# Kernel tuning notes

Hardware: AMD Instinct MI355X
Metric: run time of the kernel (lower is better)

The kernel has to match this reference:

```python
import jax, jax.numpy as jnp
import numpy as np

B = 2; D0 = 41; H = 200; W = 176
C_IN = 128; C_MID = 64
N_PER = 15000; N = B * N_PER
EPS = 1e-3  # spconv BatchNorm1d eps=0.001


def bn_relu(x, valid, gamma, beta):
    # BatchNorm1d (training mode) over ACTIVE voxels only, then ReLU; invalid rows zeroed
    m = valid.astype(x.dtype)[:, None]
    cnt = jnp.maximum(m.sum(), 1.0)
    mean = (x * m).sum(0) / cnt
    var = (((x - mean) ** 2) * m).sum(0) / cnt
    y = gamma * (x - mean) * jax.lax.rsqrt(var + EPS) + beta
    return jnp.maximum(y, 0.0) * m


def build_idx_map(coords, valid, D):
    # dense voxel -> row-index map (-1 = inactive); invalid rows routed out-of-bounds and dropped
    n = coords.shape[0]
    oob = jnp.array([B, D, H, W], jnp.int32)
    c = jnp.where(valid[:, None], coords, oob)
    idx = jnp.full((B, D, H, W), -1, jnp.int32)
    return idx.at[c[:, 0], c[:, 1], c[:, 2], c[:, 3]].set(
        jnp.arange(n, dtype=jnp.int32), mode='drop')


def subm_conv3(feats, coords, valid, idx_map, weight):
    # submanifold 3x3x3 conv: gather active neighbors, GEMM per kernel offset, accumulate
    D = idx_map.shape[1]
    b, z, y, x = coords[:, 0], coords[:, 1], coords[:, 2], coords[:, 3]
    out = jnp.zeros((feats.shape[0], weight.shape[-1]), feats.dtype)
    for dz in (-1, 0, 1):
        for dy in (-1, 0, 1):
            for dx in (-1, 0, 1):
                nz, ny, nx = z + dz, y + dy, x + dx
                inb = valid & (nz >= 0) & (nz < D) & (ny >= 0) & (ny < H) \
                      & (nx >= 0) & (nx < W)
                j = idx_map[b, jnp.clip(nz, 0, D - 1),
                            jnp.clip(ny, 0, H - 1), jnp.clip(nx, 0, W - 1)]
                ok = inb & (j >= 0)
                g = jnp.where(ok[:, None], feats[jnp.clip(j, 0)], 0.0)
                out = out + g @ weight[dz + 1, dy + 1, dx + 1]
    return out


def sparse_conv_z(feats, coords, valid, D, weight):
    # regular SparseConv3d kernel (3,1,1), stride (2,1,1), pad 0: scatter-GEMM into unique outputs
    Dout = (D - 3) // 2 + 1
    b, z, y, x = coords[:, 0], coords[:, 1], coords[:, 2], coords[:, 3]
    sent = B * Dout * H * W  # sentinel linear id (> any valid id)
    cap = 2 * feats.shape[0] + 1  # each input hits <= 2 outputs, + sentinel slot
    lins, vals = [], []
    for kz in range(3):
        t = z - kz
        oz = t // 2
        ok = valid & (t >= 0) & (t % 2 == 0) & (oz < Dout)
        lin = ((b * Dout + oz) * H + y) * W + x
        lins.append(jnp.where(ok, lin, sent))
        vals.append(feats @ weight[kz])
    lin_all = jnp.concatenate(lins)
    val_all = jnp.concatenate(vals)
    uniq = jnp.unique(lin_all, size=cap, fill_value=sent)
    seg = jnp.searchsorted(uniq, lin_all)
    out = jax.ops.segment_sum(val_all, seg, num_segments=cap)
    new_valid = uniq != sent
    lin = jnp.where(new_valid, uniq, 0)
    nb = lin // (Dout * H * W)
    r = lin % (Dout * H * W)
    nz = r // (H * W)
    ny = (r % (H * W)) // W
    nx = r % W
    new_coords = jnp.stack([nb, nz, ny, nx], 1).astype(jnp.int32)
    return out, new_coords, new_valid, Dout


def forward(voxel_features, coors, batch_size,
            w_subm0, g0, b0, w_s1, gs1, bs1,
            w_subm1a, g1a, b1a, w_subm1b, g1b, b1b, w_s2, gs2, bs2):
    v0 = jnp.ones((voxel_features.shape[0],), bool)
    idx0 = build_idx_map(coors, v0, D0)
    x = subm_conv3(voxel_features, coors, v0, idx0, w_subm0)   # 128 -> 64, subm0
    x = bn_relu(x, v0, g0, b0)
    x, c1, v1, D1 = sparse_conv_z(x, coors, v0, D0, w_s1)      # D: 41 -> 20
    x = bn_relu(x, v1, gs1, bs1)
    idx1 = build_idx_map(c1, v1, D1)
    x = bn_relu(subm_conv3(x, c1, v1, idx1, w_subm1a), v1, g1a, b1a)  # subm1
    x = bn_relu(subm_conv3(x, c1, v1, idx1, w_subm1b), v1, g1b, b1b)
    x, c2, v2, D2 = sparse_conv_z(x, c1, v1, D1, w_s2)         # D: 20 -> 9
    x = bn_relu(x, v2, gs2, bs2)
    oob = jnp.array([B, D2, H, W], jnp.int32)
    c2s = jnp.where(v2[:, None], c2, oob)
    dense = jnp.zeros((B, D2, H, W, C_MID), x.dtype)
    dense = dense.at[c2s[:, 0], c2s[:, 1], c2s[:, 2], c2s[:, 3]].set(x, mode='drop')
    dense = dense.transpose(0, 4, 1, 2, 3)                     # [B, C, D2, H, W]
    return dense.reshape(B, C_MID * D2, H, W)


def setup_inputs() -> dict:
    key = jax.random.key(0)
    ks = jax.random.split(key, 6)
    rng = np.random.default_rng(0)
    rows = []
    for b in range(B):
        lin = rng.choice(D0 * H * W, N_PER, replace=False)
        z = lin // (H * W); y = (lin % (H * W)) // W; x = lin % W
        rows.append(np.stack([np.full(N_PER, b), z, y, x], 1))
    coors = jnp.asarray(np.concatenate(rows), jnp.int32)
    s0 = 1.0 / np.sqrt(27.0 * C_IN)
    s1 = 1.0 / np.sqrt(27.0 * C_MID)
    sz = 1.0 / np.sqrt(3.0 * C_MID)
    ones = jnp.ones((C_MID,), jnp.float32)
    zeros = jnp.zeros((C_MID,), jnp.float32)
    return {
        'voxel_features': jax.random.normal(ks[0], (N, C_IN), jnp.float32),
        'coors': coors,
        'batch_size': B,
        'w_subm0': jax.random.normal(ks[1], (3, 3, 3, C_IN, C_MID), jnp.float32) * s0,
        'g0': ones, 'b0': zeros,
        'w_s1': jax.random.normal(ks[2], (3, C_MID, C_MID), jnp.float32) * sz,
        'gs1': ones, 'bs1': zeros,
        'w_subm1a': jax.random.normal(ks[3], (3, 3, 3, C_MID, C_MID), jnp.float32) * s1,
        'g1a': ones, 'b1a': zeros,
        'w_subm1b': jax.random.normal(ks[4], (3, 3, 3, C_MID, C_MID), jnp.float32) * s1,
        'g1b': ones, 'b1b': zeros,
        'w_s2': jax.random.normal(ks[5], (3, C_MID, C_MID), jnp.float32) * sz,
        'gs2': ones, 'bs2': zeros,
    }


def reference(voxel_features, coors, batch_size,
              w_subm0, g0, b0, w_s1, gs1, bs1,
              w_subm1a, g1a, b1a, w_subm1b, g1b, b1b, w_s2, gs2, bs2):
    return forward(voxel_features, coors, batch_size,
                   w_subm0, g0, b0, w_s1, gs1, bs1,
                   w_subm1a, g1a, b1a, w_subm1b, g1b, b1b, w_s2, gs2, bs2)
```

## Files before the change

### kernel.cpp

```cpp
#include <hip/hip_runtime.h>

typedef unsigned short u16;
typedef unsigned int u32;
typedef unsigned long long u64;
typedef __attribute__((ext_vector_type(8))) short bf16x8;
typedef __attribute__((ext_vector_type(4))) float f32x4;

#define H_ 200
#define W_ 176
#define HW_ (200 * 176)
#define D0_ 41
#define D1_ 20
#define D2_ 9
#define B_ 2

__device__ __forceinline__ u16 f2bf(float f) {
  union { float f; u32 u; } c; c.f = f;
  u32 u = c.u;
  u32 r = (u + 0x7fffu + ((u >> 16) & 1u)) >> 16;
  return (u16)r;
}

__global__ void k_boot1(int* __restrict__ ctrl, float* __restrict__ stats,
                        uint4* __restrict__ fillp, int nfill16, int N) {
  int t = blockIdx.x * 256 + threadIdx.x;
  if (t < nfill16) {
    uint4 v;
    v.x = 0xFFFFFFFFu; v.y = 0xFFFFFFFFu; v.z = 0xFFFFFFFFu; v.w = 0xFFFFFFFFu;
    fillp[t] = v;
    return;
  }
  t -= nfill16;
  if (t < 3) ctrl[t] = (t == 0) ? N : 0;
  else if (t < 3 + 2560) stats[t - 3] = 0.f;
}

__device__ __forceinline__ void repack1(const float* __restrict__ w, u16* __restrict__ frag,
                                        int K, int t) {
  int j = t & 7;
  int lane = (t >> 3) & 63;
  int nt = (t >> 9) & 3;
  int rest = t >> 11;
  int KS = K / 32;
  int ks = rest % KS;
  int o = rest / KS;
  int k = ks * 32 + (lane >> 4) * 8 + j;
  int n = nt * 16 + (lane & 15);
  frag[t] = f2bf(w[((size_t)o * K + k) * 64 + n]);
}

__global__ void k_boot2(const float* __restrict__ feats, const float* __restrict__ w0s,
                        const float* __restrict__ w1as, const float* __restrict__ w1bs,
                        const float* __restrict__ wz1s, const float* __restrict__ wz2s,
                        const int* __restrict__ coors,
                        u16* __restrict__ fb, u16* __restrict__ wf0, u16* __restrict__ wf1a,
                        u16* __restrict__ wf1b, u16* __restrict__ wfz1, u16* __restrict__ wfz2,
                        int* __restrict__ idx0, int N) {
  int t = blockIdx.x * 256 + threadIdx.x;
  int NC = N * 128;
  if (t < NC) { fb[t] = f2bf(feats[t]); return; }
  t -= NC;
  if (t < 221184) { repack1(w0s, wf0, 128, t); return; }
  t -= 221184;
  if (t < 110592) { repack1(w1as, wf1a, 64, t); return; }
  t -= 110592;
  if (t < 110592) { repack1(w1bs, wf1b, 64, t); return; }
  t -= 110592;
  if (t < 12288) { repack1(wz1s, wfz1, 64, t); return; }
  t -= 12288;
  if (t < 12288) { repack1(wz2s, wfz2, 64, t); return; }
  t -= 12288;
  if (t < N) {
    int b = coors[t * 4], z = coors[t * 4 + 1], y = coors[t * 4 + 2], x = coors[t * 4 + 3];
    idx0[((size_t)(b * D0_ + z) * H_ + y) * W_ + x] = t;
  }
}

__device__ __forceinline__ void claim_ep(int t, int base64, int cnt,
                                         const int* __restrict__ coordsIn,
                                         const int* __restrict__ idxin, int Din, int Dout,
                                         int* __restrict__ claim, int* __restrict__ coords_out,
                                         int* __restrict__ nbrzN, int* __restrict__ outcnt) {
  int i = base64 + t;
  bool w0 = false, w1 = false;
  int pos0 = 0, pos1 = 0, oz0 = -1, oz1 = -1;
  int b = 0, z = 0, yy = 0, xx = 0;
  if (i < cnt) {
    int4 cc = *(const int4*)(coordsIn + (size_t)i * 4);
    b = cc.x; z = cc.y; yy = cc.z; xx = cc.w;
    if (z & 1) {
      int oz = (z - 1) >> 1;
      if (oz < Dout) oz0 = oz;
    } else {
      int oz = z >> 1;
      if (oz < Dout) oz0 = oz;
      if (z >= 2) oz1 = oz - 1;
    }
    if (oz0 >= 0) {
      pos0 = ((b * Dout + oz0) * H_ + yy) * W_ + xx;
      w0 = (atomicCAS(&claim[pos0], -1, -2) == -1);
    }
    if (oz1 >= 0) {
      pos1 = ((b * Dout + oz1) * H_ + yy) * W_ + xx;
      w1 = (atomicCAS(&claim[pos1], -1, -2) == -1);
    }
  }
  u64 m0 = __ballot(w0), m1 = __ballot(w1);
  int c0 = __popcll(m0), c1 = __popcll(m1);
  int lane = t & 63;
  u64 lt = (lane == 63) ? 0x7FFFFFFFFFFFFFFFull : ((1ull << lane) - 1ull);
  int bse2 = 0;
  if (lane == 0 && (c0 + c1) > 0) bse2 = atomicAdd(outcnt, c0 + c1);
  bse2 = __shfl(bse2, 0);
  if (w0) {
    int id = bse2 + __popcll(m0 & lt);
    claim[pos0] = id;
    coords_out[id * 4 + 0] = b; coords_out[id * 4 + 1] = oz0;
    coords_out[id * 4 + 2] = yy; coords_out[id * 4 + 3] = xx;
    size_t bse = ((size_t)(b * Din + 2 * oz0) * H_ + yy) * W_ + xx;
    nbrzN[id * 3 + 0] = idxin[bse];
    nbrzN[id * 3 + 1] = idxin[bse + HW_];
    nbrzN[id * 3 + 2] = idxin[bse + 2 * (size_t)HW_];
  }
  if (w1) {
    int id = bse2 + c0 + __popcll(m1 & lt);
    claim[pos1] = id;
    coords_out[id * 4 + 0] = b; coords_out[id * 4 + 1] = oz1;
    coords_out[id * 4 + 2] = yy; coords_out[id * 4 + 3] = xx;
    size_t bse = ((size_t)(b * Din + 2 * oz1) * H_ + yy) * W_ + xx;
    nbrzN[id * 3 + 0] = idxin[bse];
    nbrzN[id * 3 + 1] = idxin[bse + HW_];
    nbrzN[id * 3 + 2] = idxin[bse + 2 * (size_t)HW_];
  }
}

__global__ __launch_bounds__(256) void k_conv0(const u16* __restrict__ feats,
                                               const int* __restrict__ coords,
                                               const int* __restrict__ idxmap,
                                               const u16* __restrict__ wfrag,
                                               float* __restrict__ out, int cnt,
                                               float* __restrict__ statsL,
                                               int* __restrict__ claim, int* __restrict__ coords_out,
                                               int* __restrict__ nbrzN, int* __restrict__ outcnt) {
  constexpr int KS = 4;
  __shared__ int snbr[1728];
  __shared__ u32 smask[4];
  __shared__ float lsum[64], lss[64];
  int t = threadIdx.x;
  if (t < 64) { lsum[t] = 0.f; lss[t] = 0.f; }
  if (t < 4) smask[t] = 0;
  __syncthreads();
  int blockBase = blockIdx.x * 64;
  for (int r = t; r < 1728; r += 256) {
    int g = r / 432;
    int rr = r - g * 432;
    int o = rr >> 4;
    int i = blockBase + g * 16 + (rr & 15);
    int j = -1;
    if (i < cnt) {
      int4 cc = *(const int4*)(coords + (size_t)i * 4);
      int nz = cc.y + o / 9 - 1, ny = cc.z + (o / 3) % 3 - 1, nx = cc.w + o % 3 - 1;
      if ((u32)nz < (u32)D0_ && (u32)ny < (u32)H_ && (u32)nx < (u32)W_)
        j = idxmap[((size_t)(cc.x * D0_ + nz) * H_ + ny) * W_ + nx];
    }
    snbr[r] = j;
    if (j >= 0) atomicOr(&smask[g], 1u << o);
  }
  __syncthreads();
  int lane = t & 63;
  int wg = t >> 6;
  int base = blockBase + wg * 16;
  int am = lane & 15, kr = lane >> 4;
  f32x4 acc0 = {0.f, 0.f, 0.f, 0.f};
  f32x4 acc1 = acc0, acc2 = acc0, acc3 = acc0;
  if (base < cnt) {
    u32 mask = smask[wg];
    const int* nb = snbr + wg * 432 + am;
    bf16x8 zf = {0, 0, 0, 0, 0, 0, 0, 0};
    bf16x8 a[KS], an[KS];
    if (mask) {
      int o = __builtin_ctz(mask); mask &= mask - 1;
      int j = nb[o * 16];
#pragma unroll
      for (int ks = 0; ks < KS; ++ks)
        a[ks] = (j >= 0) ? *(const bf16x8*)(feats + (size_t)j * 128 + ks * 32 + kr * 8) : zf;
      while (true) {
        int on = -1, jn = -1;
        if (mask) { on = __builtin_ctz(mask); mask &= mask - 1; jn = nb[on * 16]; }
#pragma unroll
        for (int ks = 0; ks < KS; ++ks)
          an[ks] = (jn >= 0) ? *(const bf16x8*)(feats + (size_t)jn * 128 + ks * 32 + kr * 8) : zf;
        const u16* bw = wfrag + (size_t)o * (KS * 2048) + lane * 8;
#pragma unroll
        for (int ks = 0; ks < KS; ++ks) {
          const u16* bwk = bw + ks * 2048;
          acc0 = __builtin_amdgcn_mfma_f32_16x16x32_bf16(a[ks], *(const bf16x8*)(bwk), acc0, 0, 0, 0);
          acc1 = __builtin_amdgcn_mfma_f32_16x16x32_bf16(a[ks], *(const bf16x8*)(bwk + 512), acc1, 0, 0, 0);
          acc2 = __builtin_amdgcn_mfma_f32_16x16x32_bf16(a[ks], *(const bf16x8*)(bwk + 1024), acc2, 0, 0, 0);
          acc3 = __builtin_amdgcn_mfma_f32_16x16x32_bf16(a[ks], *(const bf16x8*)(bwk + 1536), acc3, 0, 0, 0);
        }
        if (on < 0) break;
        o = on;
#pragma unroll
        for (int ks = 0; ks < KS; ++ks) a[ks] = an[ks];
      }
    }
    float s0 = 0.f, s1 = 0.f, s2 = 0.f, s3 = 0.f;
    float q0 = 0.f, q1 = 0.f, q2 = 0.f, q3 = 0.f;
#pragma unroll
    for (int r = 0; r < 4; ++r) {
      int po = base + kr * 4 + r;
      if (po < cnt) {
        float* op = out + (size_t)po * 64 + am;
        op[0] = acc0[r]; op[16] = acc1[r]; op[32] = acc2[r]; op[48] = acc3[r];
        s0 += acc0[r]; q0 += acc0[r] * acc0[r];
        s1 += acc1[r]; q1 += acc1[r] * acc1[r];
        s2 += acc2[r]; q2 += acc2[r] * acc2[r];
        s3 += acc3[r]; q3 += acc3[r] * acc3[r];
      }
    }
    atomicAdd(&lsum[am], s0); atomicAdd(&lss[am], q0);
    atomicAdd(&lsum[am + 16], s1); atomicAdd(&lss[am + 16], q1);
    atomicAdd(&lsum[am + 32], s2); atomicAdd(&lss[am + 32], q2);
    atomicAdd(&lsum[am + 48], s3); atomicAdd(&lss[am + 48], q3);
  }
  __syncthreads();
  if (t < 64) {
    float s = lsum[t], q = lss[t];
    if (s != 0.f || q != 0.f) {
      float* dst = statsL + (blockIdx.x & 3) * 128;
      atomicAdd(&dst[t], s);
      atomicAdd(&dst[64 + t], q);
    }
    claim_ep(t, blockBase, cnt, coords, idxmap, D0_, D1_, claim, coords_out, nbrzN, outcnt);
  }
}

__device__ __forceinline__ void bn_pre(const float* __restrict__ statsIn, int cntN,
                                       const float* __restrict__ gamma,
                                       const float* __restrict__ beta,
                                       float* __restrict__ ggs, float* __restrict__ bbs, int t) {
  if (t < 64) {
    float s = 0.f, q = 0.f;
#pragma unroll
    for (int k = 0; k < 4; ++k) { s += statsIn[k * 128 + t]; q += statsIn[k * 128 + 64 + t]; }
    float cf = (float)(cntN > 0 ? cntN : 1);
    float mean = s / cf;
    float var = q / cf - mean * mean;
    float inv = rsqrtf(var + 1e-3f);
    float g = gamma[t] * inv;
    ggs[t] = g;
    bbs[t] = beta[t] - mean * g;
  }
}

__global__ __launch_bounds__(256) void k_convz(
    const float* __restrict__ xp, const int* __restrict__ nbrz_in,
    const u16* __restrict__ wfrag, const float* __restrict__ statsIn,
    const int* __restrict__ cntNormP, const float* __restrict__ gamma,
    const float* __restrict__ beta, float* __restrict__ out, const int* __restrict__ cntp,
    float* __restrict__ statsOut,
    const int* __restrict__ coordsL, const int* __restrict__ idxL, int DL,
    int* __restrict__ nbrT, u32* __restrict__ gmaskT,
    int Dnext, int* __restrict__ claimN, int* __restrict__ coordsN,
    int* __restrict__ nbrzN, int* __restrict__ cntN2) {
  int cnt = *cntp;
  int blockBase = blockIdx.x * 64;
  if (blockBase >= cnt) return;
  __shared__ float lsum[64], lss[64], ggs[64], bbs[64];
  __shared__ u32 smask[4];
  int t = threadIdx.x;
  if (t < 64) { lsum[t] = 0.f; lss[t] = 0.f; }
  if (t < 4) smask[t] = 0;
  bn_pre(statsIn, *cntNormP, gamma, beta, ggs, bbs, t);
  __syncthreads();
  if (nbrT) {
    for (int r = t; r < 1728; r += 256) {
      int g = r / 432;
      int rr = r - g * 432;
      int o = rr >> 4;
      int i = blockBase + g * 16 + (rr & 15);
      int j = -1;
      if (i < cnt) {
        int4 cc = *(const int4*)(coordsL + (size_t)i * 4);
        int nz = cc.y + o / 9 - 1, ny = cc.z + (o / 3) % 3 - 1, nx = cc.w + o % 3 - 1;
        if ((u32)nz < (u32)DL && (u32)ny < (u32)H_ && (u32)nx < (u32)W_)
          j = idxL[((size_t)(cc.x * DL + nz) * H_ + ny) * W_ + nx];
      }
      nbrT[(size_t)(blockIdx.x * 4 + g) * 432 + rr] = j;
      if (j >= 0) atomicOr(&smask[g], 1u << o);
    }
  }
  int lane = t & 63;
  int wg = t >> 6;
  int base = blockBase + wg * 16;
  int am = lane & 15, kr = lane >> 4;
  float gr_[16], br_[16];
#pragma unroll
  for (int ks = 0; ks < 2; ++ks)
#pragma unroll
    for (int e = 0; e < 8; ++e) {
      int c = ks * 32 + kr * 8 + e;
      gr_[ks * 8 + e] = ggs[c];
      br_[ks * 8 + e] = bbs[c];
    }
  f32x4 acc0 = {0.f, 0.f, 0.f, 0.f};
  f32x4 acc1 = acc0, acc2 = acc0, acc3 = acc0;
  if (base < cnt) {
    int pt = base + am;
    bool vpt = pt < cnt;
    const int* np = nbrz_in + (size_t)pt * 3;
    bf16x8 zf = {0, 0, 0, 0, 0, 0, 0, 0};
    bf16x8 a[2], an[2];
    auto buildA = [&](int j, bf16x8* aa) {
      if (j >= 0) {
        const float* src = xp + (size_t)j * 64 + kr * 8;
#pragma unroll
        for (int ks = 0; ks < 2; ++ks) {
          float4 v0 = *(const float4*)(src + ks * 32);
          float4 v1 = *(const float4*)(src + ks * 32 + 4);
          bf16x8 w;
          w[0] = (short)f2bf(fmaxf(v0.x * gr_[ks * 8 + 0] + br_[ks * 8 + 0], 0.f));
          w[1] = (short)f2bf(fmaxf(v0.y * gr_[ks * 8 + 1] + br_[ks * 8 + 1], 0.f));
          w[2] = (short)f2bf(fmaxf(v0.z * gr_[ks * 8 + 2] + br_[ks * 8 + 2], 0.f));
          w[3] = (short)f2bf(fmaxf(v0.w * gr_[ks * 8 + 3] + br_[ks * 8 + 3], 0.f));
          w[4] = (short)f2bf(fmaxf(v1.x * gr_[ks * 8 + 4] + br_[ks * 8 + 4], 0.f));
          w[5] = (short)f2bf(fmaxf(v1.y * gr_[ks * 8 + 5] + br_[ks * 8 + 5], 0.f));
          w[6] = (short)f2bf(fmaxf(v1.z * gr_[ks * 8 + 6] + br_[ks * 8 + 6], 0.f));
          w[7] = (short)f2bf(fmaxf(v1.w * gr_[ks * 8 + 7] + br_[ks * 8 + 7], 0.f));
          aa[ks] = w;
        }
      } else { aa[0] = zf; aa[1] = zf; }
    };
    int j = vpt ? np[0] : -1;
    buildA(j, a);
    for (int o = 0; o < 3; ++o) {
      int jn = (o + 1 < 3 && vpt) ? np[o + 1] : -1;
      buildA(jn, an);
      const u16* bw = wfrag + (size_t)o * 4096 + lane * 8;
#pragma unroll
      for (int ks = 0; ks < 2; ++ks) {
        const u16* bwk = bw + ks * 2048;
        acc0 = __builtin_amdgcn_mfma_f32_16x16x32_bf16(a[ks], *(const bf16x8*)(bwk), acc0, 0, 0, 0);
        acc1 = __builtin_amdgcn_mfma_f32_16x16x32_bf16(a[ks], *(const bf16x8*)(bwk + 512), acc1, 0, 0, 0);
        acc2 = __builtin_amdgcn_mfma_f32_16x16x32_bf16(a[ks], *(const bf16x8*)(bwk + 1024), acc2, 0, 0, 0);
        acc3 = __builtin_amdgcn_mfma_f32_16x16x32_bf16(a[ks], *(const bf16x8*)(bwk + 1536), acc3, 0, 0, 0);
      }
      a[0] = an[0]; a[1] = an[1];
    }
    float s0 = 0.f, s1 = 0.f, s2 = 0.f, s3 = 0.f;
    float q0 = 0.f, q1 = 0.f, q2 = 0.f, q3 = 0.f;
#pragma unroll
    for (int r = 0; r < 4; ++r) {
      int po = base + kr * 4 + r;
      if (po < cnt) {
        float* op = out + (size_t)po * 64 + am;
        op[0] = acc0[r]; op[16] = acc1[r]; op[32] = acc2[r]; op[48] = acc3[r];
        s0 += acc0[r]; q0 += acc0[r] * acc0[r];
        s1 += acc1[r]; q1 += acc1[r] * acc1[r];
        s2 += acc2[r]; q2 += acc2[r] * acc2[r];
        s3 += acc3[r]; q3 += acc3[r] * acc3[r];
      }
    }
    atomicAdd(&lsum[am], s0); atomicAdd(&lss[am], q0);
    atomicAdd(&lsum[am + 16], s1); atomicAdd(&lss[am + 16], q1);
    atomicAdd(&lsum[am + 32], s2); atomicAdd(&lss[am + 32], q2);
    atomicAdd(&lsum[am + 48], s3); atomicAdd(&lss[am + 48], q3);
  }
  __syncthreads();
  if (nbrT && t < 4) gmaskT[blockIdx.x * 4 + t] = smask[t];
  if (t < 64) {
    float s = lsum[t], q = lss[t];
    if (s != 0.f || q != 0.f) {
      float* dst = statsOut + (blockIdx.x & 3) * 128;
      atomicAdd(&dst[t], s);
      atomicAdd(&dst[64 + t], q);
    }
    if (claimN)
      claim_ep(t, blockBase, cnt, coordsL, idxL, DL, Dnext, claimN, coordsN, nbrzN, cntN2);
  }
}

__global__ __launch_bounds__(256) void k_conv1(
    const float* __restrict__ xp, const int* __restrict__ nbrT, const u32* __restrict__ gmaskT,
    const u16* __restrict__ wfrag, const float* __restrict__ statsIn,
    const int* __restrict__ cntNormP, const float* __restrict__ gamma,
    const float* __restrict__ beta, float* __restrict__ out, const int* __restrict__ cntp,
    float* __restrict__ statsOut) {
  int cnt = *cntp;
  int blockBase = blockIdx.x * 64;
  if (blockBase >= cnt) return;
  __shared__ float lsum[64], lss[64], ggs[64], bbs[64];
  int t = threadIdx.x;
  if (t < 64) { lsum[t] = 0.f; lss[t] = 0.f; }
  bn_pre(statsIn, *cntNormP, gamma, beta, ggs, bbs, t);
  __syncthreads();
  int lane = t & 63;
  int wg = t >> 6;
  int g = blockIdx.x * 4 + wg;
  int base = blockBase + wg * 16;
  int am = lane & 15, kr = lane >> 4;
  float gr_[16], br_[16];
#pragma unroll
  for (int ks = 0; ks < 2; ++ks)
#pragma unroll
    for (int e = 0; e < 8; ++e) {
      int c = ks * 32 + kr * 8 + e;
      gr_[ks * 8 + e] = ggs[c];
      br_[ks * 8 + e] = bbs[c];
    }
  f32x4 acc0 = {0.f, 0.f, 0.f, 0.f};
  f32x4 acc1 = acc0, acc2 = acc0, acc3 = acc0;
  if (base < cnt) {
    u32 mask = gmaskT[g];
    const int* nb = nbrT + (size_t)g * 432 + am;
    bf16x8 zf = {0, 0, 0, 0, 0, 0, 0, 0};
    bf16x8 a[2], an[2];
    auto buildA = [&](int j, bf16x8* aa) {
      if (j >= 0) {
        const float* src = xp + (size_t)j * 64 + kr * 8;
#pragma unroll
        for (int ks = 0; ks < 2; ++ks) {
          float4 v0 = *(const float4*)(src + ks * 32);
          float4 v1 = *(const float4*)(src + ks * 32 + 4);
          bf16x8 w;
          w[0] = (short)f2bf(fmaxf(v0.x * gr_[ks * 8 + 0] + br_[ks * 8 + 0], 0.f));
          w[1] = (short)f2bf(fmaxf(v0.y * gr_[ks * 8 + 1] + br_[ks * 8 + 1], 0.f));
          w[2] = (short)f2bf(fmaxf(v0.z * gr_[ks * 8 + 2] + br_[ks * 8 + 2], 0.f));
          w[3] = (short)f2bf(fmaxf(v0.w * gr_[ks * 8 + 3] + br_[ks * 8 + 3], 0.f));
          w[4] = (short)f2bf(fmaxf(v1.x * gr_[ks * 8 + 4] + br_[ks * 8 + 4], 0.f));
          w[5] = (short)f2bf(fmaxf(v1.y * gr_[ks * 8 + 5] + br_[ks * 8 + 5], 0.f));
          w[6] = (short)f2bf(fmaxf(v1.z * gr_[ks * 8 + 6] + br_[ks * 8 + 6], 0.f));
          w[7] = (short)f2bf(fmaxf(v1.w * gr_[ks * 8 + 7] + br_[ks * 8 + 7], 0.f));
          aa[ks] = w;
        }
      } else { aa[0] = zf; aa[1] = zf; }
    };
    if (mask) {
      int o = __builtin_ctz(mask); mask &= mask - 1;
      int j = nb[o * 16];
      buildA(j, a);
      while (true) {
        int on = -1, jn = -1;
        if (mask) { on = __builtin_ctz(mask); mask &= mask - 1; jn = nb[on * 16]; }
        buildA(jn, an);
        const u16* bw = wfrag + (size_t)o * 4096 + lane * 8;
#pragma unroll
        for (int ks = 0; ks < 2; ++ks) {
          const u16* bwk = bw + ks * 2048;
          acc0 = __builtin_amdgcn_mfma_f32_16x16x32_bf16(a[ks], *(const bf16x8*)(bwk), acc0, 0, 0, 0);
          acc1 = __builtin_amdgcn_mfma_f32_16x16x32_bf16(a[ks], *(const bf16x8*)(bwk + 512), acc1, 0, 0, 0);
          acc2 = __builtin_amdgcn_mfma_f32_16x16x32_bf16(a[ks], *(const bf16x8*)(bwk + 1024), acc2, 0, 0, 0);
          acc3 = __builtin_amdgcn_mfma_f32_16x16x32_bf16(a[ks], *(const bf16x8*)(bwk + 1536), acc3, 0, 0, 0);
        }
        if (on < 0) break;
        o = on;
        a[0] = an[0]; a[1] = an[1];
      }
    }
    float s0 = 0.f, s1 = 0.f, s2 = 0.f, s3 = 0.f;
    float q0 = 0.f, q1 = 0.f, q2 = 0.f, q3 = 0.f;
#pragma unroll
    for (int r = 0; r < 4; ++r) {
      int po = base + kr * 4 + r;
      if (po < cnt) {
        float* op = out + (size_t)po * 64 + am;
        op[0] = acc0[r]; op[16] = acc1[r]; op[32] = acc2[r]; op[48] = acc3[r];
        s0 += acc0[r]; q0 += acc0[r] * acc0[r];
        s1 += acc1[r]; q1 += acc1[r] * acc1[r];
        s2 += acc2[r]; q2 += acc2[r] * acc2[r];
        s3 += acc3[r]; q3 += acc3[r] * acc3[r];
      }
    }
    atomicAdd(&lsum[am], s0); atomicAdd(&lss[am], q0);
    atomicAdd(&lsum[am + 16], s1); atomicAdd(&lss[am + 16], q1);
    atomicAdd(&lsum[am + 32], s2); atomicAdd(&lss[am + 32], q2);
    atomicAdd(&lsum[am + 48], s3); atomicAdd(&lss[am + 48], q3);
  }
  __syncthreads();
  if (t < 64) {
    float s = lsum[t], q = lss[t];
    if (s != 0.f || q != 0.f) {
      float* dst = statsOut + (blockIdx.x & 3) * 128;
      atomicAdd(&dst[t], s);
      atomicAdd(&dst[64 + t], q);
    }
  }
}

__global__ void k_output(const float* __restrict__ x, const int* __restrict__ cntp,
                         const float* __restrict__ stats, const float* __restrict__ gamma,
                         const float* __restrict__ beta, const int* __restrict__ claim2,
                         float* __restrict__ out) {
  const int XQ = W_ / 4;
  int t = blockIdx.x * 256 + threadIdx.x;
  int total = B_ * 64 * D2_ * H_ * XQ;
  if (t >= total) return;
  int xq = t % XQ;
  int row = t / XQ;
  int y = row % H_;
  int r2 = row / H_;
  int oz = r2 % D2_;
  r2 /= D2_;
  int c = r2 & 63;
  int b = r2 >> 6;
  int cnt = *cntp;
  float s = 0.f, q = 0.f;
#pragma unroll
  for (int k = 0; k < 4; ++k) { s += stats[k * 128 + c]; q += stats[k * 128 + 64 + c]; }
  float cf = (float)(cnt > 0 ? cnt : 1);
  float mean = s / cf;
  float var = q / cf - mean * mean;
  float inv = rsqrtf(var + 1e-3f);
  float g = gamma[c] * inv;
  float bb = beta[c] - mean * g;
  int pos = ((b * D2_ + oz) * H_ + y) * W_ + xq * 4;
  int4 ids = *(const int4*)(claim2 + pos);
  float4 v;
  v.x = (ids.x >= 0) ? fmaxf(x[(size_t)ids.x * 64 + c] * g + bb, 0.f) : 0.f;
  v.y = (ids.y >= 0) ? fmaxf(x[(size_t)ids.y * 64 + c] * g + bb, 0.f) : 0.f;
  v.z = (ids.z >= 0) ? fmaxf(x[(size_t)ids.z * 64 + c] * g + bb, 0.f) : 0.f;
  v.w = (ids.w >= 0) ? fmaxf(x[(size_t)ids.w * 64 + c] * g + bb, 0.f) : 0.f;
  *(float4*)(out + (size_t)row * W_ + xq * 4) = v;
}

extern "C" void kernel_launch(void* const* d_in, const int* in_sizes, int n_in,
                              void* d_out, int out_size, void* d_ws, size_t ws_size,
                              hipStream_t stream) {
  const int N = in_sizes[0] / 128;
  const int cap1 = 2 * N + 8;
  const int cap2 = 4 * N + 8;
  const int ng1 = (cap1 + 15) / 16;

  char* ws = (char*)d_ws;
  size_t off = 0;
  auto alloc = [&](size_t bytes) -> void* {
    size_t o = off;
    off = (off + bytes + 255) & ~(size_t)255;
    return (void*)(ws + o);
  };

  int* ctrl = (int*)alloc(16);
  float* stats = (float*)alloc(2560 * 4);
  size_t fill_beg = off;
  int* idx0 = (int*)alloc((size_t)B_ * D0_ * HW_ * 4);
  int* idx1 = (int*)alloc((size_t)B_ * D1_ * HW_ * 4);
  int* claim2 = (int*)alloc((size_t)B_ * D2_ * HW_ * 4);
  size_t fill_end = off;
  int* nbr1 = (int*)alloc((size_t)(ng1 + 4) * 432 * 4);
  u32* gmask1 = (u32*)alloc((size_t)(ng1 + 4) * 4);
  int* nbrz1 = (int*)alloc((size_t)cap1 * 3 * 4);
  int* nbrz2 = (int*)alloc((size_t)cap2 * 3 * 4);
  int* coords1 = (int*)alloc((size_t)cap1 * 4 * 4);
  int* coords2 = (int*)alloc((size_t)cap2 * 4 * 4);
  float* xb0 = (float*)alloc((size_t)N * 64 * 4);
  float* xb1 = (float*)alloc((size_t)cap1 * 64 * 4);
  float* xb2 = (float*)alloc((size_t)cap1 * 64 * 4);
  float* xb3 = (float*)alloc((size_t)cap1 * 64 * 4);
  float* xb4 = (float*)alloc((size_t)cap2 * 64 * 4);
  u16* fb = (u16*)alloc((size_t)N * 128 * 2);
  u16* wf0 = (u16*)alloc((size_t)27 * 4 * 2048 * 2);
  u16* wf1a = (u16*)alloc((size_t)27 * 2 * 2048 * 2);
  u16* wf1b = (u16*)alloc((size_t)27 * 2 * 2048 * 2);
  u16* wfz1 = (u16*)alloc((size_t)3 * 2 * 2048 * 2);
  u16* wfz2 = (u16*)alloc((size_t)3 * 2 * 2048 * 2);

  const int* coors = (const int*)d_in[1];
  auto gr = [](long n) { return dim3((unsigned)((n + 255) / 256)); };

  int nfill16 = (int)((fill_end - fill_beg) / 16);
  k_boot1<<<gr((long)nfill16 + 2563), 256, 0, stream>>>(ctrl, stats,
                                                        (uint4*)(ws + fill_beg), nfill16, N);
  long prepTotal = (long)N * 128 + 221184 + 110592 + 110592 + 12288 + 12288 + N;
  k_boot2<<<gr(prepTotal), 256, 0, stream>>>((const float*)d_in[0], (const float*)d_in[3],
                                             (const float*)d_in[9], (const float*)d_in[12],
                                             (const float*)d_in[6], (const float*)d_in[15],
                                             coors, fb, wf0, wf1a, wf1b, wfz1, wfz2, idx0, N);
  k_conv0<<<dim3((N + 63) / 64), 256, 0, stream>>>(fb, coors, idx0, wf0, xb0, N, stats + 0,
                                                   idx1, coords1, nbrz1, ctrl + 1);
  k_convz<<<dim3((cap1 + 63) / 64), 256, 0, stream>>>(
      xb0, nbrz1, wfz1, stats + 0, ctrl + 0, (const float*)d_in[4], (const float*)d_in[5],
      xb1, ctrl + 1, stats + 512,
      coords1, idx1, D1_, nbr1, gmask1,
      D2_, claim2, coords2, nbrz2, ctrl + 2);
  k_conv1<<<dim3((cap1 + 63) / 64), 256, 0, stream>>>(
      xb1, nbr1, gmask1, wf1a, stats + 512, ctrl + 1, (const float*)d_in[7],
      (const float*)d_in[8], xb2, ctrl + 1, stats + 1024);
  k_conv1<<<dim3((cap1 + 63) / 64), 256, 0, stream>>>(
      xb2, nbr1, gmask1, wf1b, stats + 1024, ctrl + 1, (const float*)d_in[10],
      (const float*)d_in[11], xb3, ctrl + 1, stats + 1536);
  k_convz<<<dim3((cap2 + 63) / 64), 256, 0, stream>>>(
      xb3, nbrz2, wfz2, stats + 1536, ctrl + 1, (const float*)d_in[13], (const float*)d_in[14],
      xb4, ctrl + 2, stats + 2048,
      nullptr, nullptr, 0, nullptr, nullptr,
      0, nullptr, nullptr, nullptr, nullptr);
  long outThreads = (long)B_ * 64 * D2_ * H_ * (W_ / 4);
  k_output<<<gr(outThreads), 256, 0, stream>>>(xb4, ctrl + 2, stats + 2048,
                                               (const float*)d_in[16], (const float*)d_in[17],
                                               claim2, (float*)d_out);
}
```

Baseline: 381.9 us.

## Fuse all pipeline stages into one cooperative persistent kernel with grid syncs

Replaces the chain of seven separate kernel launches with a single cooperative kernel of 256 persistent blocks that walks each stage in grid-stride loops, separated by grid.sync barriers. A fallback path launches per-stage kernels if the cooperative launch fails. The aim is to remove kernel launch gaps and tail drain between stages. The cost is a fixed 256-block grid with one block per CU, which lowers occupancy and latency hiding in the gather-heavy conv stages, plus the overhead of each grid barrier.

New measurement: 1.074 ms. 2.81x slower.

```diff
diff --git a/kernel.cpp b/kernel.cpp
--- a/kernel.cpp
+++ b/kernel.cpp
@@ -1,4 +1,7 @@
 #include <hip/hip_runtime.h>
+#include <hip/hip_cooperative_groups.h>
+
+namespace cg = cooperative_groups;
 
 typedef unsigned short u16;
 typedef unsigned int u32;
@@ -13,6 +16,7 @@
 #define D1_ 20
 #define D2_ 9
 #define B_ 2
+#define NBLK 256
 
 __device__ __forceinline__ u16 f2bf(float f) {
   union { float f; u32 u; } c; c.f = f;
@@ -21,19 +25,27 @@
   return (u16)r;
 }
 
-__global__ void k_boot1(int* __restrict__ ctrl, float* __restrict__ stats,
-                        uint4* __restrict__ fillp, int nfill16, int N) {
-  int t = blockIdx.x * 256 + threadIdx.x;
-  if (t < nfill16) {
-    uint4 v;
-    v.x = 0xFFFFFFFFu; v.y = 0xFFFFFFFFu; v.z = 0xFFFFFFFFu; v.w = 0xFFFFFFFFu;
-    fillp[t] = v;
-    return;
-  }
-  t -= nfill16;
-  if (t < 3) ctrl[t] = (t == 0) ? N : 0;
-  else if (t < 3 + 2560) stats[t - 3] = 0.f;
-}
+struct P {
+  const float* feats; const int* coors;
+  const float *w0, *w1a, *w1b, *wz1, *wz2;
+  const float *g0, *b0, *g1, *b1, *g2, *b2, *g3, *b3, *g4, *b4;
+  int* ctrl; float* stats;
+  int *idx0, *idx1, *claim2;
+  int* nbr1; u32* gmask1;
+  int *nbrz1, *nbrz2, *coords1, *coords2;
+  float *xb0, *xb1, *xb2, *xb3, *xb4;
+  u16 *fb, *wf0, *wf1a, *wf1b, *wfz1, *wfz2;
+  float* out;
+  uint4* fillp;
+  int N, nfill16;
+  long prepTotal;
+};
+
+struct SMem {
+  int snbr[1728];
+  u32 smask[4];
+  float lsum[64], lss[64], ggs[64], bbs[64];
+};
 
 __device__ __forceinline__ void repack1(const float* __restrict__ w, u16* __restrict__ frag,
                                         int K, int t) {
@@ -49,30 +61,24 @@
   frag[t] = f2bf(w[((size_t)o * K + k) * 64 + n]);
 }
 
-__global__ void k_boot2(const float* __restrict__ feats, const float* __restrict__ w0s,
-                        const float* __restrict__ w1as, const float* __restrict__ w1bs,
-                        const float* __restrict__ wz1s, const float* __restrict__ wz2s,
-                        const int* __restrict__ coors,
-                        u16* __restrict__ fb, u16* __restrict__ wf0, u16* __restrict__ wf1a,
-                        u16* __restrict__ wf1b, u16* __restrict__ wfz1, u16* __restrict__ wfz2,
-                        int* __restrict__ idx0, int N) {
-  int t = blockIdx.x * 256 + threadIdx.x;
-  int NC = N * 128;
-  if (t < NC) { fb[t] = f2bf(feats[t]); return; }
-  t -= NC;
-  if (t < 221184) { repack1(w0s, wf0, 128, t); return; }
-  t -= 221184;
-  if (t < 110592) { repack1(w1as, wf1a, 64, t); return; }
-  t -= 110592;
-  if (t < 110592) { repack1(w1bs, wf1b, 64, t); return; }
-  t -= 110592;
-  if (t < 12288) { repack1(wz1s, wfz1, 64, t); return; }
-  t -= 12288;
-  if (t < 12288) { repack1(wz2s, wfz2, 64, t); return; }
-  t -= 12288;
-  if (t < N) {
-    int b = coors[t * 4], z = coors[t * 4 + 1], y = coors[t * 4 + 2], x = coors[t * 4 + 3];
-    idx0[((size_t)(b * D0_ + z) * H_ + y) * W_ + x] = t;
+__device__ __forceinline__ void prep_one(const P& p, long tt) {
+  long NC = (long)p.N * 128;
+  if (tt < NC) { p.fb[tt] = f2bf(p.feats[tt]); return; }
+  tt -= NC;
+  if (tt < 221184) { repack1(p.w0, p.wf0, 128, (int)tt); return; }
+  tt -= 221184;
+  if (tt < 110592) { repack1(p.w1a, p.wf1a, 64, (int)tt); return; }
+  tt -= 110592;
+  if (tt < 110592) { repack1(p.w1b, p.wf1b, 64, (int)tt); return; }
+  tt -= 110592;
+  if (tt < 12288) { repack1(p.wz1, p.wfz1, 64, (int)tt); return; }
+  tt -= 12288;
+  if (tt < 12288) { repack1(p.wz2, p.wfz2, 64, (int)tt); return; }
+  tt -= 12288;
+  if (tt < p.N) {
+    int i = (int)tt;
+    int b = p.coors[i * 4], z = p.coors[i * 4 + 1], y = p.coors[i * 4 + 2], x = p.coors[i * 4 + 3];
+    p.idx0[((size_t)(b * D0_ + z) * H_ + y) * W_ + x] = i;
   }
 }
 
@@ -134,108 +140,6 @@
   }
 }
 
-__global__ __launch_bounds__(256) void k_conv0(const u16* __restrict__ feats,
-                                               const int* __restrict__ coords,
-                                               const int* __restrict__ idxmap,
-                                               const u16* __restrict__ wfrag,
-                                               float* __restrict__ out, int cnt,
-                                               float* __restrict__ statsL,
-                                               int* __restrict__ claim, int* __restrict__ coords_out,
-                                               int* __restrict__ nbrzN, int* __restrict__ outcnt) {
-  constexpr int KS = 4;
-  __shared__ int snbr[1728];
-  __shared__ u32 smask[4];
-  __shared__ float lsum[64], lss[64];
-  int t = threadIdx.x;
-  if (t < 64) { lsum[t] = 0.f; lss[t] = 0.f; }
-  if (t < 4) smask[t] = 0;
-  __syncthreads();
-  int blockBase = blockIdx.x * 64;
-  for (int r = t; r < 1728; r += 256) {
-    int g = r / 432;
-    int rr = r - g * 432;
-    int o = rr >> 4;
-    int i = blockBase + g * 16 + (rr & 15);
-    int j = -1;
-    if (i < cnt) {
-      int4 cc = *(const int4*)(coords + (size_t)i * 4);
-      int nz = cc.y + o / 9 - 1, ny = cc.z + (o / 3) % 3 - 1, nx = cc.w + o % 3 - 1;
-      if ((u32)nz < (u32)D0_ && (u32)ny < (u32)H_ && (u32)nx < (u32)W_)
-        j = idxmap[((size_t)(cc.x * D0_ + nz) * H_ + ny) * W_ + nx];
-    }
-    snbr[r] = j;
-    if (j >= 0) atomicOr(&smask[g], 1u << o);
-  }
-  __syncthreads();
-  int lane = t & 63;
-  int wg = t >> 6;
-  int base = blockBase + wg * 16;
-  int am = lane & 15, kr = lane >> 4;
-  f32x4 acc0 = {0.f, 0.f, 0.f, 0.f};
-  f32x4 acc1 = acc0, acc2 = acc0, acc3 = acc0;
-  if (base < cnt) {
-    u32 mask = smask[wg];
-    const int* nb = snbr + wg * 432 + am;
-    bf16x8 zf = {0, 0, 0, 0, 0, 0, 0, 0};
-    bf16x8 a[KS], an[KS];
-    if (mask) {
-      int o = __builtin_ctz(mask); mask &= mask - 1;
-      int j = nb[o * 16];
-#pragma unroll
-      for (int ks = 0; ks < KS; ++ks)
-        a[ks] = (j >= 0) ? *(const bf16x8*)(feats + (size_t)j * 128 + ks * 32 + kr * 8) : zf;
-      while (true) {
-        int on = -1, jn = -1;
-        if (mask) { on = __builtin_ctz(mask); mask &= mask - 1; jn = nb[on * 16]; }
-#pragma unroll
-        for (int ks = 0; ks < KS; ++ks)
-          an[ks] = (jn >= 0) ? *(const bf16x8*)(feats + (size_t)jn * 128 + ks * 32 + kr * 8) : zf;
-        const u16* bw = wfrag + (size_t)o * (KS * 2048) + lane * 8;
-#pragma unroll
-        for (int ks = 0; ks < KS; ++ks) {
-          const u16* bwk = bw + ks * 2048;
-          acc0 = __builtin_amdgcn_mfma_f32_16x16x32_bf16(a[ks], *(const bf16x8*)(bwk), acc0, 0, 0, 0);
-          acc1 = __builtin_amdgcn_mfma_f32_16x16x32_bf16(a[ks], *(const bf16x8*)(bwk + 512), acc1, 0, 0, 0);
-          acc2 = __builtin_amdgcn_mfma_f32_16x16x32_bf16(a[ks], *(const bf16x8*)(bwk + 1024), acc2, 0, 0, 0);
-          acc3 = __builtin_amdgcn_mfma_f32_16x16x32_bf16(a[ks], *(const bf16x8*)(bwk + 1536), acc3, 0, 0, 0);
-        }
-        if (on < 0) break;
-        o = on;
-#pragma unroll
-        for (int ks = 0; ks < KS; ++ks) a[ks] = an[ks];
-      }
-    }
-    float s0 = 0.f, s1 = 0.f, s2 = 0.f, s3 = 0.f;
-    float q0 = 0.f, q1 = 0.f, q2 = 0.f, q3 = 0.f;
-#pragma unroll
-    for (int r = 0; r < 4; ++r) {
-      int po = base + kr * 4 + r;
-      if (po < cnt) {
-        float* op = out + (size_t)po * 64 + am;
-        op[0] = acc0[r]; op[16] = acc1[r]; op[32] = acc2[r]; op[48] = acc3[r];
-        s0 += acc0[r]; q0 += acc0[r] * acc0[r];
-        s1 += acc1[r]; q1 += acc1[r] * acc1[r];
-        s2 += acc2[r]; q2 += acc2[r] * acc2[r];
-        s3 += acc3[r]; q3 += acc3[r] * acc3[r];
-      }
-    }
-    atomicAdd(&lsum[am], s0); atomicAdd(&lss[am], q0);
-    atomicAdd(&lsum[am + 16], s1); atomicAdd(&lss[am + 16], q1);
-    atomicAdd(&lsum[am + 32], s2); atomicAdd(&lss[am + 32], q2);
-    atomicAdd(&lsum[am + 48], s3); atomicAdd(&lss[am + 48], q3);
-  }
-  __syncthreads();
-  if (t < 64) {
-    float s = lsum[t], q = lss[t];
-    if (s != 0.f || q != 0.f) {
-      float* dst = statsL + (blockIdx.x & 3) * 128;
-      atomicAdd(&dst[t], s);
-      atomicAdd(&dst[64 + t], q);
-    }
-    claim_ep(t, blockBase, cnt, coords, idxmap, D0_, D1_, claim, coords_out, nbrzN, outcnt);
-  }
-}
-
 __device__ __forceinline__ void bn_pre(const float* __restrict__ statsIn, int cntN,
                                        const float* __restrict__ gamma,
                                        const float* __restrict__ beta,
@@ -254,27 +158,105 @@
   }
 }
 
-__global__ __launch_bounds__(256) void k_convz(
-    const float* __restrict__ xp, const int* __restrict__ nbrz_in,
-    const u16* __restrict__ wfrag, const float* __restrict__ statsIn,
-    const int* __restrict__ cntNormP, const float* __restrict__ gamma,
-    const float* __restrict__ beta, float* __restrict__ out, const int* __restrict__ cntp,
-    float* __restrict__ statsOut,
-    const int* __restrict__ coordsL, const int* __restrict__ idxL, int DL,
-    int* __restrict__ nbrT, u32* __restrict__ gmaskT,
-    int Dnext, int* __restrict__ claimN, int* __restrict__ coordsN,
-    int* __restrict__ nbrzN, int* __restrict__ cntN2) {
-  int cnt = *cntp;
-  int blockBase = blockIdx.x * 64;
-  if (blockBase >= cnt) return;
-  __shared__ float lsum[64], lss[64], ggs[64], bbs[64];
-  __shared__ u32 smask[4];
-  int t = threadIdx.x;
-  if (t < 64) { lsum[t] = 0.f; lss[t] = 0.f; }
-  if (t < 4) smask[t] = 0;
-  bn_pre(statsIn, *cntNormP, gamma, beta, ggs, bbs, t);
-  __syncthreads();
-  if (nbrT) {
+__device__ __forceinline__ void buildA64(const float* __restrict__ xp, int j, int kr,
+                                         const float* gr_, const float* br_, bf16x8* aa) {
+  if (j >= 0) {
+    const float* src = xp + (size_t)j * 64 + kr * 8;
+#pragma unroll
+    for (int ks = 0; ks < 2; ++ks) {
+      float4 v0 = *(const float4*)(src + ks * 32);
+      float4 v1 = *(const float4*)(src + ks * 32 + 4);
+      bf16x8 w;
+      w[0] = (short)f2bf(fmaxf(v0.x * gr_[ks * 8 + 0] + br_[ks * 8 + 0], 0.f));
+      w[1] = (short)f2bf(fmaxf(v0.y * gr_[ks * 8 + 1] + br_[ks * 8 + 1], 0.f));
+      w[2] = (short)f2bf(fmaxf(v0.z * gr_[ks * 8 + 2] + br_[ks * 8 + 2], 0.f));
+      w[3] = (short)f2bf(fmaxf(v0.w * gr_[ks * 8 + 3] + br_[ks * 8 + 3], 0.f));
+      w[4] = (short)f2bf(fmaxf(v1.x * gr_[ks * 8 + 4] + br_[ks * 8 + 4], 0.f));
+      w[5] = (short)f2bf(fmaxf(v1.y * gr_[ks * 8 + 5] + br_[ks * 8 + 5], 0.f));
+      w[6] = (short)f2bf(fmaxf(v1.z * gr_[ks * 8 + 6] + br_[ks * 8 + 6], 0.f));
+      w[7] = (short)f2bf(fmaxf(v1.w * gr_[ks * 8 + 7] + br_[ks * 8 + 7], 0.f));
+      aa[ks] = w;
+    }
+  } else {
+    bf16x8 zf = {0, 0, 0, 0, 0, 0, 0, 0};
+    aa[0] = zf; aa[1] = zf;
+  }
+}
+
+template <int KS>
+__device__ __forceinline__ void mfma_step(const u16* __restrict__ bw, const bf16x8* a,
+                                          f32x4& acc0, f32x4& acc1, f32x4& acc2, f32x4& acc3) {
+#pragma unroll
+  for (int ks = 0; ks < KS; ++ks) {
+    const u16* bwk = bw + ks * 2048;
+    acc0 = __builtin_amdgcn_mfma_f32_16x16x32_bf16(a[ks], *(const bf16x8*)(bwk), acc0, 0, 0, 0);
+    acc1 = __builtin_amdgcn_mfma_f32_16x16x32_bf16(a[ks], *(const bf16x8*)(bwk + 512), acc1, 0, 0, 0);
+    acc2 = __builtin_amdgcn_mfma_f32_16x16x32_bf16(a[ks], *(const bf16x8*)(bwk + 1024), acc2, 0, 0, 0);
+    acc3 = __builtin_amdgcn_mfma_f32_16x16x32_bf16(a[ks], *(const bf16x8*)(bwk + 1536), acc3, 0, 0, 0);
+  }
+}
+
+__device__ __forceinline__ void store_stats(int base, int cnt, int am, int kr,
+                                            const f32x4& acc0, const f32x4& acc1,
+                                            const f32x4& acc2, const f32x4& acc3,
+                                            float* __restrict__ out,
+                                            float* __restrict__ lsum, float* __restrict__ lss) {
+  float s0 = 0.f, s1 = 0.f, s2 = 0.f, s3 = 0.f;
+  float q0 = 0.f, q1 = 0.f, q2 = 0.f, q3 = 0.f;
+#pragma unroll
+  for (int r = 0; r < 4; ++r) {
+    int po = base + kr * 4 + r;
+    if (po < cnt) {
+      float* op = out + (size_t)po * 64 + am;
+      op[0] = acc0[r]; op[16] = acc1[r]; op[32] = acc2[r]; op[48] = acc3[r];
+      s0 += acc0[r]; q0 += acc0[r] * acc0[r];
+      s1 += acc1[r]; q1 += acc1[r] * acc1[r];
+      s2 += acc2[r]; q2 += acc2[r] * acc2[r];
+      s3 += acc3[r]; q3 += acc3[r] * acc3[r];
+    }
+  }
+  atomicAdd(&lsum[am], s0); atomicAdd(&lss[am], q0);
+  atomicAdd(&lsum[am + 16], s1); atomicAdd(&lss[am + 16], q1);
+  atomicAdd(&lsum[am + 32], s2); atomicAdd(&lss[am + 32], q2);
+  atomicAdd(&lsum[am + 48], s3); atomicAdd(&lss[am + 48], q3);
+}
+
+__device__ __forceinline__ void flush_stats(int t, int bid, float* __restrict__ statsOut,
+                                            const float* __restrict__ lsum,
+                                            const float* __restrict__ lss) {
+  if (t < 64) {
+    float s = lsum[t], q = lss[t];
+    if (s != 0.f || q != 0.f) {
+      float* dst = statsOut + (bid & 3) * 128;
+      atomicAdd(&dst[t], s);
+      atomicAdd(&dst[64 + t], q);
+    }
+  }
+}
+
+
+__device__ void stage0(const P& p, long gtid, long gstride) {
+  uint4 v;
+  v.x = 0xFFFFFFFFu; v.y = 0xFFFFFFFFu; v.z = 0xFFFFFFFFu; v.w = 0xFFFFFFFFu;
+  for (long i = gtid; i < p.nfill16; i += gstride) p.fillp[i] = v;
+  for (long i = gtid; i < 2560; i += gstride) p.stats[i] = 0.f;
+  if (gtid < 3) p.ctrl[gtid] = (gtid == 0) ? p.N : 0;
+}
+
+__device__ void stage1(const P& p, long gtid, long gstride) {
+  for (long tt = gtid; tt < p.prepTotal; tt += gstride) prep_one(p, tt);
+}
+
+__device__ void stage2(const P& p, SMem* sm, int bid, int gsz, int t) {
+  const int cnt = p.N;
+  const int lane = t & 63, wg = t >> 6, am = lane & 15, kr = lane >> 4;
+  if (t < 64) { sm->lsum[t] = 0.f; sm->lss[t] = 0.f; }
+  const int nblk = (cnt + 63) / 64;
+  for (int blk = bid; blk < nblk; blk += gsz) {
+    __syncthreads();
+    if (t < 4) sm->smask[t] = 0;
+    __syncthreads();
+    int blockBase = blk * 64;
     for (int r = t; r < 1728; r += 256) {
       int g = r / 432;
       int rr = r - g * 432;
@@ -282,247 +264,282 @@
       int i = blockBase + g * 16 + (rr & 15);
       int j = -1;
       if (i < cnt) {
-        int4 cc = *(const int4*)(coordsL + (size_t)i * 4);
+        int4 cc = *(const int4*)(p.coors + (size_t)i * 4);
         int nz = cc.y + o / 9 - 1, ny = cc.z + (o / 3) % 3 - 1, nx = cc.w + o % 3 - 1;
-        if ((u32)nz < (u32)DL && (u32)ny < (u32)H_ && (u32)nx < (u32)W_)
-          j = idxL[((size_t)(cc.x * DL + nz) * H_ + ny) * W_ + nx];
+        if ((u32)nz < (u32)D0_ && (u32)ny < (u32)H_ && (u32)nx < (u32)W_)
+          j = p.idx0[((size_t)(cc.x * D0_ + nz) * H_ + ny) * W_ + nx];
       }
-      nbrT[(size_t)(blockIdx.x * 4 + g) * 432 + rr] = j;
-      if (j >= 0) atomicOr(&smask[g], 1u << o);
-    }
-  }
-  int lane = t & 63;
-  int wg = t >> 6;
-  int base = blockBase + wg * 16;
-  int am = lane & 15, kr = lane >> 4;
+      sm->snbr[r] = j;
+      if (j >= 0) atomicOr(&sm->smask[g], 1u << o);
+    }
+    __syncthreads();
+    int base = blockBase + wg * 16;
+    f32x4 acc0 = {0.f, 0.f, 0.f, 0.f};
+    f32x4 acc1 = acc0, acc2 = acc0, acc3 = acc0;
+    if (base < cnt) {
+      u32 mask = sm->smask[wg];
+      const int* nb = sm->snbr + wg * 432 + am;
+      bf16x8 zf = {0, 0, 0, 0, 0, 0, 0, 0};
+      bf16x8 a[4], an[4];
+      if (mask) {
+        int o = __builtin_ctz(mask); mask &= mask - 1;
+        int j = nb[o * 16];
+#pragma unroll
+        for (int ks = 0; ks < 4; ++ks)
+          a[ks] = (j >= 0) ? *(const bf16x8*)(p.fb + (size_t)j * 128 + ks * 32 + kr * 8) : zf;
+        while (true) {
+          int on = -1, jn = -1;
+          if (mask) { on = __builtin_ctz(mask); mask &= mask - 1; jn = nb[on * 16]; }
+#pragma unroll
+          for (int ks = 0; ks < 4; ++ks)
+            an[ks] = (jn >= 0) ? *(const bf16x8*)(p.fb + (size_t)jn * 128 + ks * 32 + kr * 8) : zf;
+          mfma_step<4>(p.wf0 + (size_t)o * 8192 + lane * 8, a, acc0, acc1, acc2, acc3);
+          if (on < 0) break;
+          o = on;
+#pragma unroll
+          for (int ks = 0; ks < 4; ++ks) a[ks] = an[ks];
+        }
+      }
+      store_stats(base, cnt, am, kr, acc0, acc1, acc2, acc3, p.xb0, sm->lsum, sm->lss);
+    }
+    if (t < 64)
+      claim_ep(t, blockBase, cnt, p.coors, p.idx0, D0_, D1_, p.idx1, p.coords1, p.nbrz1,
+               p.ctrl + 1);
+  }
+  __syncthreads();
+  flush_stats(t, bid, p.stats + 0, sm->lsum, sm->lss);
+}
+
+__device__ void stage3(const P& p, SMem* sm, int bid, int gsz, int t) {
+  const int cnt1 = p.ctrl[1];
+  const int nblk1 = (cnt1 + 63) / 64;
+  const int lane = t & 63, wg = t >> 6, am = lane & 15, kr = lane >> 4;
+  if (t < 64) { sm->lsum[t] = 0.f; sm->lss[t] = 0.f; }
+  bn_pre(p.stats + 0, p.N, p.g0, p.b0, sm->ggs, sm->bbs, t);
+  __syncthreads();
   float gr_[16], br_[16];
 #pragma unroll
   for (int ks = 0; ks < 2; ++ks)
 #pragma unroll
     for (int e = 0; e < 8; ++e) {
       int c = ks * 32 + kr * 8 + e;
-      gr_[ks * 8 + e] = ggs[c];
-      br_[ks * 8 + e] = bbs[c];
-    }
-  f32x4 acc0 = {0.f, 0.f, 0.f, 0.f};
-  f32x4 acc1 = acc0, acc2 = acc0, acc3 = acc0;
-  if (base < cnt) {
-    int pt = base + am;
-    bool vpt = pt < cnt;
-    const int* np = nbrz_in + (size_t)pt * 3;
-    bf16x8 zf = {0, 0, 0, 0, 0, 0, 0, 0};
-    bf16x8 a[2], an[2];
-    auto buildA = [&](int j, bf16x8* aa) {
-      if (j >= 0) {
-        const float* src = xp + (size_t)j * 64 + kr * 8;
-#pragma unroll
-        for (int ks = 0; ks < 2; ++ks) {
-          float4 v0 = *(const float4*)(src + ks * 32);
-          float4 v1 = *(const float4*)(src + ks * 32 + 4);
-          bf16x8 w;
-          w[0] = (short)f2bf(fmaxf(v0.x * gr_[ks * 8 + 0] + br_[ks * 8 + 0], 0.f));
-          w[1] = (short)f2bf(fmaxf(v0.y * gr_[ks * 8 + 1] + br_[ks * 8 + 1], 0.f));
-          w[2] = (short)f2bf(fmaxf(v0.z * gr_[ks * 8 + 2] + br_[ks * 8 + 2], 0.f));
-          w[3] = (short)f2bf(fmaxf(v0.w * gr_[ks * 8 + 3] + br_[ks * 8 + 3], 0.f));
-          w[4] = (short)f2bf(fmaxf(v1.x * gr_[ks * 8 + 4] + br_[ks * 8 + 4], 0.f));
-          w[5] = (short)f2bf(fmaxf(v1.y * gr_[ks * 8 + 5] + br_[ks * 8 + 5], 0.f));
-          w[6] = (short)f2bf(fmaxf(v1.z * gr_[ks * 8 + 6] + br_[ks * 8 + 6], 0.f));
-          w[7] = (short)f2bf(fmaxf(v1.w * gr_[ks * 8 + 7] + br_[ks * 8 + 7], 0.f));
-          aa[ks] = w;
-        }
-      } else { aa[0] = zf; aa[1] = zf; }
-    };
-    int j = vpt ? np[0] : -1;
-    buildA(j, a);
-    for (int o = 0; o < 3; ++o) {
-      int jn = (o + 1 < 3 && vpt) ? np[o + 1] : -1;
-      buildA(jn, an);
-      const u16* bw = wfrag + (size_t)o * 4096 + lane * 8;
-#pragma unroll
-      for (int ks = 0; ks < 2; ++ks) {
-        const u16* bwk = bw + ks * 2048;
-        acc0 = __builtin_amdgcn_mfma_f32_16x16x32_bf16(a[ks], *(const bf16x8*)(bwk), acc0, 0, 0, 0);
-        acc1 = __builtin_amdgcn_mfma_f32_16x16x32_bf16(a[ks], *(const bf16x8*)(bwk + 512), acc1, 0, 0, 0);
-        acc2 = __builtin_amdgcn_mfma_f32_16x16x32_bf16(a[ks], *(const bf16x8*)(bwk + 1024), acc2, 0, 0, 0);
-        acc3 = __builtin_amdgcn_mfma_f32_16x16x32_bf16(a[ks], *(const bf16x8*)(bwk + 1536), acc3, 0, 0, 0);
+      gr_[ks * 8 + e] = sm->ggs[c];
+      br_[ks * 8 + e] = sm->bbs[c];
+    }
+  for (int blk = bid; blk < nblk1; blk += gsz) {
+    __syncthreads();
+    if (t < 4) sm->smask[t] = 0;
+    __syncthreads();
+    int blockBase = blk * 64;
+    for (int r = t; r < 1728; r += 256) {
+      int g = r / 432;
+      int rr = r - g * 432;
+      int o = rr >> 4;
+      int i = blockBase + g * 16 + (rr & 15);
+      int j = -1;
+      if (i < cnt1) {
+        int4 cc = *(const int4*)(p.coords1 + (size_t)i * 4);
+        int nz = cc.y + o / 9 - 1, ny = cc.z + (o / 3) % 3 - 1, nx = cc.w + o % 3 - 1;
+        if ((u32)nz < (u32)D1_ && (u32)ny < (u32)H_ && (u32)nx < (u32)W_)
+          j = p.idx1[((size_t)(cc.x * D1_ + nz) * H_ + ny) * W_ + nx];
       }
-      a[0] = an[0]; a[1] = an[1];
-    }
-    float s0 = 0.f, s1 = 0.f, s2 = 0.f, s3 = 0.f;
-    float q0 = 0.f, q1 = 0.f, q2 = 0.f, q3 = 0.f;
-#pragma unroll
-    for (int r = 0; r < 4; ++r) {
-      int po = base + kr * 4 + r;
-      if (po < cnt) {
-        float* op = out + (size_t)po * 64 + am;
-        op[0] = acc0[r]; op[16] = acc1[r]; op[32] = acc2[r]; op[48] = acc3[r];
-        s0 += acc0[r]; q0 += acc0[r] * acc0[r];
-        s1 += acc1[r]; q1 += acc1[r] * acc1[r];
-        s2 += acc2[r]; q2 += acc2[r] * acc2[r];
-        s3 += acc3[r]; q3 += acc3[r] * acc3[r];
+      p.nbr1[(size_t)(blk * 4 + g) * 432 + rr] = j;
+      if (j >= 0) atomicOr(&sm->smask[g], 1u << o);
+    }
+    __syncthreads();
+    if (t < 4) p.gmask1[blk * 4 + t] = sm->smask[t];
+    int base = blockBase + wg * 16;
+    f32x4 acc0 = {0.f, 0.f, 0.f, 0.f};
+    f32x4 acc1 = acc0, acc2 = acc0, acc3 = acc0;
+    if (base < cnt1) {
+      int pt = base + am;
+      bool vpt = pt < cnt1;
+      const int* np = p.nbrz1 + (size_t)pt * 3;
+      bf16x8 a[2], an[2];
+      int j = vpt ? np[0] : -1;
+      buildA64(p.xb0, j, kr, gr_, br_, a);
+      for (int o = 0; o < 3; ++o) {
+        int jn = (o + 1 < 3 && vpt) ? np[o + 1] : -1;
+        buildA64(p.xb0, jn, kr, gr_, br_, an);
+        mfma_step<2>(p.wfz1 + (size_t)o * 4096 + lane * 8, a, acc0, acc1, acc2, acc3);
+        a[0] = an[0]; a[1] = an[1];
       }
-    }
-    atomicAdd(&lsum[am], s0); atomicAdd(&lss[am], q0);
-    atomicAdd(&lsum[am + 16], s1); atomicAdd(&lss[am + 16], q1);
-    atomicAdd(&lsum[am + 32], s2); atomicAdd(&lss[am + 32], q2);
-    atomicAdd(&lsum[am + 48], s3); atomicAdd(&lss[am + 48], q3);
+      store_stats(base, cnt1, am, kr, acc0, acc1, acc2, acc3, p.xb1, sm->lsum, sm->lss);
+    }
+    if (t < 64)
+      claim_ep(t, blockBase, cnt1, p.coords1, p.idx1, D1_, D2_, p.claim2, p.coords2, p.nbrz2,
+               p.ctrl + 2);
   }
   __syncthreads();
-  if (nbrT && t < 4) gmaskT[blockIdx.x * 4 + t] = smask[t];
-  if (t < 64) {
-    float s = lsum[t], q = lss[t];
-    if (s != 0.f || q != 0.f) {
-      float* dst = statsOut + (blockIdx.x & 3) * 128;
-      atomicAdd(&dst[t], s);
-      atomicAdd(&dst[64 + t], q);
-    }
-    if (claimN)
-      claim_ep(t, blockBase, cnt, coordsL, idxL, DL, Dnext, claimN, coordsN, nbrzN, cntN2);
-  }
-}
-
-__global__ __launch_bounds__(256) void k_conv1(
-    const float* __restrict__ xp, const int* __restrict__ nbrT, const u32* __restrict__ gmaskT,
-    const u16* __restrict__ wfrag, const float* __restrict__ statsIn,
-    const int* __restrict__ cntNormP, const float* __restrict__ gamma,
-    const float* __restrict__ beta, float* __restrict__ out, const int* __restrict__ cntp,
-    float* __restrict__ statsOut) {
-  int cnt = *cntp;
-  int blockBase = blockIdx.x * 64;
-  if (blockBase >= cnt) return;
-  __shared__ float lsum[64], lss[64], ggs[64], bbs[64];
-  int t = threadIdx.x;
-  if (t < 64) { lsum[t] = 0.f; lss[t] = 0.f; }
-  bn_pre(statsIn, *cntNormP, gamma, beta, ggs, bbs, t);
+  flush_stats(t, bid, p.stats + 512, sm->lsum, sm->lss);
+}
+
+__device__ void stage45(const P& p, SMem* sm, int bid, int gsz, int t, int s) {
+  const int cnt1 = p.ctrl[1];
+  const int nblk1 = (cnt1 + 63) / 64;
+  const int lane = t & 63, wg = t >> 6, am = lane & 15, kr = lane >> 4;
+  const float* xin = s ? p.xb2 : p.xb1;
+  float* xout = s ? p.xb3 : p.xb2;
+  const u16* wf = s ? p.wf1b : p.wf1a;
+  const float* sIn = s ? (p.stats + 1024) : (p.stats + 512);
+  float* sOut = s ? (p.stats + 1536) : (p.stats + 1024);
+  const float* gam = s ? p.g2 : p.g1;
+  const float* bet = s ? p.b2 : p.b1;
+  if (t < 64) { sm->lsum[t] = 0.f; sm->lss[t] = 0.f; }
+  bn_pre(sIn, cnt1, gam, bet, sm->ggs, sm->bbs, t);
   __syncthreads();
-  int lane = t & 63;
-  int wg = t >> 6;
-  int g = blockIdx.x * 4 + wg;
-  int base = blockBase + wg * 16;
-  int am = lane & 15, kr = lane >> 4;
   float gr_[16], br_[16];
 #pragma unroll
   for (int ks = 0; ks < 2; ++ks)
 #pragma unroll
     for (int e = 0; e < 8; ++e) {
       int c = ks * 32 + kr * 8 + e;
-      gr_[ks * 8 + e] = ggs[c];
-      br_[ks * 8 + e] = bbs[c];
-    }
-  f32x4 acc0 = {0.f, 0.f, 0.f, 0.f};
-  f32x4 acc1 = acc0, acc2 = acc0, acc3 = acc0;
-  if (base < cnt) {
-    u32 mask = gmaskT[g];
-    const int* nb = nbrT + (size_t)g * 432 + am;
-    bf16x8 zf = {0, 0, 0, 0, 0, 0, 0, 0};
+      gr_[ks * 8 + e] = sm->ggs[c];
+      br_[ks * 8 + e] = sm->bbs[c];
+    }
+  for (int blk = bid; blk < nblk1; blk += gsz) {
+    int base = blk * 64 + wg * 16;
+    if (base >= cnt1) continue;
+    int g = blk * 4 + wg;
+    u32 mask = p.gmask1[g];
+    const int* nb = p.nbr1 + (size_t)g * 432 + am;
+    f32x4 acc0 = {0.f, 0.f, 0.f, 0.f};
+    f32x4 acc1 = acc0, acc2 = acc0, acc3 = acc0;
     bf16x8 a[2], an[2];
-    auto buildA = [&](int j, bf16x8* aa) {
-      if (j >= 0) {
-        const float* src = xp + (size_t)j * 64 + kr * 8;
-#pragma unroll
-        for (int ks = 0; ks < 2; ++ks) {
-          float4 v0 = *(const float4*)(src + ks * 32);
-          float4 v1 = *(const float4*)(src + ks * 32 + 4);
-          bf16x8 w;
-          w[0] = (short)f2bf(fmaxf(v0.x * gr_[ks * 8 + 0] + br_[ks * 8 + 0], 0.f));
-          w[1] = (short)f2bf(fmaxf(v0.y * gr_[ks * 8 + 1] + br_[ks * 8 + 1], 0.f));
-          w[2] = (short)f2bf(fmaxf(v0.z * gr_[ks * 8 + 2] + br_[ks * 8 + 2], 0.f));
-          w[3] = (short)f2bf(fmaxf(v0.w * gr_[ks * 8 + 3] + br_[ks * 8 + 3], 0.f));
-          w[4] = (short)f2bf(fmaxf(v1.x * gr_[ks * 8 + 4] + br_[ks * 8 + 4], 0.f));
-          w[5] = (short)f2bf(fmaxf(v1.y * gr_[ks * 8 + 5] + br_[ks * 8 + 5], 0.f));
-          w[6] = (short)f2bf(fmaxf(v1.z * gr_[ks * 8 + 6] + br_[ks * 8 + 6], 0.f));
-          w[7] = (short)f2bf(fmaxf(v1.w * gr_[ks * 8 + 7] + br_[ks * 8 + 7], 0.f));
-          aa[ks] = w;
-        }
-      } else { aa[0] = zf; aa[1] = zf; }
-    };
     if (mask) {
       int o = __builtin_ctz(mask); mask &= mask - 1;
-      int j = nb[o * 16];
-      buildA(j, a);
+      buildA64(xin, nb[o * 16], kr, gr_, br_, a);
       while (true) {
         int on = -1, jn = -1;
         if (mask) { on = __builtin_ctz(mask); mask &= mask - 1; jn = nb[on * 16]; }
-        buildA(jn, an);
-        const u16* bw = wfrag + (size_t)o * 4096 + lane * 8;
-#pragma unroll
-        for (int ks = 0; ks < 2; ++ks) {
-          const u16* bwk = bw + ks * 2048;
-          acc0 = __builtin_amdgcn_mfma_f32_16x16x32_bf16(a[ks], *(const bf16x8*)(bwk), acc0, 0, 0, 0);
-          acc1 = __builtin_amdgcn_mfma_f32_16x16x32_bf16(a[ks], *(const bf16x8*)(bwk + 512), acc1, 0, 0, 0);
-          acc2 = __builtin_amdgcn_mfma_f32_16x16x32_bf16(a[ks], *(const bf16x8*)(bwk + 1024), acc2, 0, 0, 0);
-          acc3 = __builtin_amdgcn_mfma_f32_16x16x32_bf16(a[ks], *(const bf16x8*)(bwk + 1536), acc3, 0, 0, 0);
-        }
+        buildA64(xin, jn, kr, gr_, br_, an);
+        mfma_step<2>(wf + (size_t)o * 4096 + lane * 8, a, acc0, acc1, acc2, acc3);
         if (on < 0) break;
         o = on;
         a[0] = an[0]; a[1] = an[1];
       }
     }
-    float s0 = 0.f, s1 = 0.f, s2 = 0.f, s3 = 0.f;
-    float q0 = 0.f, q1 = 0.f, q2 = 0.f, q3 = 0.f;
-#pragma unroll
-    for (int r = 0; r < 4; ++r) {
-      int po = base + kr * 4 + r;
-      if (po < cnt) {
-        float* op = out + (size_t)po * 64 + am;
-        op[0] = acc0[r]; op[16] = acc1[r]; op[32] = acc2[r]; op[48] = acc3[r];
-        s0 += acc0[r]; q0 += acc0[r] * acc0[r];
-        s1 += acc1[r]; q1 += acc1[r] * acc1[r];
-        s2 += acc2[r]; q2 += acc2[r] * acc2[r];
-        s3 += acc3[r]; q3 += acc3[r] * acc3[r];
-      }
-    }
-    atomicAdd(&lsum[am], s0); atomicAdd(&lss[am], q0);
-    atomicAdd(&lsum[am + 16], s1); atomicAdd(&lss[am + 16], q1);
-    atomicAdd(&lsum[am + 32], s2); atomicAdd(&lss[am + 32], q2);
-    atomicAdd(&lsum[am + 48], s3); atomicAdd(&lss[am + 48], q3);
+    store_stats(base, cnt1, am, kr, acc0, acc1, acc2, acc3, xout, sm->lsum, sm->lss);
   }
   __syncthreads();
-  if (t < 64) {
-    float s = lsum[t], q = lss[t];
-    if (s != 0.f || q != 0.f) {
-      float* dst = statsOut + (blockIdx.x & 3) * 128;
-      atomicAdd(&dst[t], s);
-      atomicAdd(&dst[64 + t], q);
-    }
-  }
-}
-
-__global__ void k_output(const float* __restrict__ x, const int* __restrict__ cntp,
-                         const float* __restrict__ stats, const float* __restrict__ gamma,
-                         const float* __restrict__ beta, const int* __restrict__ claim2,
-                         float* __restrict__ out) {
+  flush_stats(t, bid, sOut, sm->lsum, sm->lss);
+}
+
+__device__ void stage6(const P& p, SMem* sm, int bid, int gsz, int t) {
+  const int cnt1 = p.ctrl[1];
+  const int cnt2 = p.ctrl[2];
+  const int lane = t & 63, wg = t >> 6, am = lane & 15, kr = lane >> 4;
+  if (t < 64) { sm->lsum[t] = 0.f; sm->lss[t] = 0.f; }
+  bn_pre(p.stats + 1536, cnt1, p.g3, p.b3, sm->ggs, sm->bbs, t);
+  __syncthreads();
+  float gr_[16], br_[16];
+#pragma unroll
+  for (int ks = 0; ks < 2; ++ks)
+#pragma unroll
+    for (int e = 0; e < 8; ++e) {
+      int c = ks * 32 + kr * 8 + e;
+      gr_[ks * 8 + e] = sm->ggs[c];
+      br_[ks * 8 + e] = sm->bbs[c];
+    }
+  const int nblk2 = (cnt2 + 63) / 64;
+  for (int blk = bid; blk < nblk2; blk += gsz) {
+    int base = blk * 64 + wg * 16;
+    if (base >= cnt2) continue;
+    int pt = base + am;
+    bool vpt = pt < cnt2;
+    const int* np = p.nbrz2 + (size_t)pt * 3;
+    f32x4 acc0 = {0.f, 0.f, 0.f, 0.f};
+    f32x4 acc1 = acc0, acc2 = acc0, acc3 = acc0;
+    bf16x8 a[2], an[2];
+    int j = vpt ? np[0] : -1;
+    buildA64(p.xb3, j, kr, gr_, br_, a);
+    for (int o = 0; o < 3; ++o) {
+      int jn = (o + 1 < 3 && vpt) ? np[o + 1] : -1;
+      buildA64(p.xb3, jn, kr, gr_, br_, an);
+      mfma_step<2>(p.wfz2 + (size_t)o * 4096 + lane * 8, a, acc0, acc1, acc2, acc3);
+      a[0] = an[0]; a[1] = an[1];
+    }
+    store_stats(base, cnt2, am, kr, acc0, acc1, acc2, acc3, p.xb4, sm->lsum, sm->lss);
+  }
+  __syncthreads();
+  flush_stats(t, bid, p.stats + 2048, sm->lsum, sm->lss);
+}
+
+__device__ void stage7(const P& p, long gtid, long gstride) {
   const int XQ = W_ / 4;
-  int t = blockIdx.x * 256 + threadIdx.x;
-  int total = B_ * 64 * D2_ * H_ * XQ;
-  if (t >= total) return;
-  int xq = t % XQ;
-  int row = t / XQ;
-  int y = row % H_;
-  int r2 = row / H_;
-  int oz = r2 % D2_;
-  r2 /= D2_;
-  int c = r2 & 63;
-  int b = r2 >> 6;
-  int cnt = *cntp;
-  float s = 0.f, q = 0.f;
-#pragma unroll
-  for (int k = 0; k < 4; ++k) { s += stats[k * 128 + c]; q += stats[k * 128 + 64 + c]; }
-  float cf = (float)(cnt > 0 ? cnt : 1);
-  float mean = s / cf;
-  float var = q / cf - mean * mean;
-  float inv = rsqrtf(var + 1e-3f);
-  float g = gamma[c] * inv;
-  float bb = beta[c] - mean * g;
-  int pos = ((b * D2_ + oz) * H_ + y) * W_ + xq * 4;
-  int4 ids = *(const int4*)(claim2 + pos);
-  float4 v;
-  v.x = (ids.x >= 0) ? fmaxf(x[(size_t)ids.x * 64 + c] * g + bb, 0.f) : 0.f;
-  v.y = (ids.y >= 0) ? fmaxf(x[(size_t)ids.y * 64 + c] * g + bb, 0.f) : 0.f;
-  v.z = (ids.z >= 0) ? fmaxf(x[(size_t)ids.z * 64 + c] * g + bb, 0.f) : 0.f;
-  v.w = (ids.w >= 0) ? fmaxf(x[(size_t)ids.w * 64 + c] * g + bb, 0.f) : 0.f;
-  *(float4*)(out + (size_t)row * W_ + xq * 4) = v;
-}
+  const int cnt2 = p.ctrl[2];
+  const long total = (long)B_ * 64 * D2_ * H_ * XQ;
+  const float* st = p.stats + 2048;
+  for (long tt = gtid; tt < total; tt += gstride) {
+    int xq = (int)(tt % XQ);
+    long row = tt / XQ;
+    int y = (int)(row % H_);
+    long r2 = row / H_;
+    int oz = (int)(r2 % D2_);
+    r2 /= D2_;
+    int c = (int)(r2 & 63);
+    int b = (int)(r2 >> 6);
+    float s = 0.f, q = 0.f;
+#pragma unroll
+    for (int k = 0; k < 4; ++k) { s += st[k * 128 + c]; q += st[k * 128 + 64 + c]; }
+    float cf = (float)(cnt2 > 0 ? cnt2 : 1);
+    float mean = s / cf;
+    float var = q / cf - mean * mean;
+    float inv = rsqrtf(var + 1e-3f);
+    float g = p.g4[c] * inv;
+    float bb = p.b4[c] - mean * g;
+    int pos = ((b * D2_ + oz) * H_ + y) * W_ + xq * 4;
+    int4 ids = *(const int4*)(p.claim2 + pos);
+    float4 v;
+    v.x = (ids.x >= 0) ? fmaxf(p.xb4[(size_t)ids.x * 64 + c] * g + bb, 0.f) : 0.f;
+    v.y = (ids.y >= 0) ? fmaxf(p.xb4[(size_t)ids.y * 64 + c] * g + bb, 0.f) : 0.f;
+    v.z = (ids.z >= 0) ? fmaxf(p.xb4[(size_t)ids.z * 64 + c] * g + bb, 0.f) : 0.f;
+    v.w = (ids.w >= 0) ? fmaxf(p.xb4[(size_t)ids.w * 64 + c] * g + bb, 0.f) : 0.f;
+    *(float4*)(p.out + (size_t)row * W_ + xq * 4) = v;
+  }
+}
+
+__global__ __launch_bounds__(256, 1) void k_mega(P p) {
+  cg::grid_group grid = cg::this_grid();
+  __shared__ SMem sm;
+  const int t = threadIdx.x;
+  const int bid = blockIdx.x;
+  const int gsz = gridDim.x;
+  const long gtid = (long)bid * 256 + t;
+  const long gstride = (long)gsz * 256;
+
+  stage0(p, gtid, gstride);
+  __threadfence();
+  grid.sync();
+  stage1(p, gtid, gstride);
+  __threadfence();
+  grid.sync();
+  stage2(p, &sm, bid, gsz, t);
+  __threadfence();
+  grid.sync();
+  stage3(p, &sm, bid, gsz, t);
+  __threadfence();
+  grid.sync();
+  stage45(p, &sm, bid, gsz, t, 0);
+  __threadfence();
+  grid.sync();
+  stage45(p, &sm, bid, gsz, t, 1);
+  __threadfence();
+  grid.sync();
+  stage6(p, &sm, bid, gsz, t);
+  __threadfence();
+  grid.sync();
+  stage7(p, gtid, gstride);
+}
+
+__global__ void k_s0(P p) { stage0(p, (long)blockIdx.x * 256 + threadIdx.x, (long)gridDim.x * 256); }
+__global__ void k_s1(P p) { stage1(p, (long)blockIdx.x * 256 + threadIdx.x, (long)gridDim.x * 256); }
+__global__ __launch_bounds__(256) void k_s2(P p) { __shared__ SMem sm; stage2(p, &sm, blockIdx.x, gridDim.x, threadIdx.x); }
+__global__ __launch_bounds__(256) void k_s3(P p) { __shared__ SMem sm; stage3(p, &sm, blockIdx.x, gridDim.x, threadIdx.x); }
+__global__ __launch_bounds__(256) void k_s4(P p) { __shared__ SMem sm; stage45(p, &sm, blockIdx.x, gridDim.x, threadIdx.x, 0); }
+__global__ __launch_bounds__(256) void k_s5(P p) { __shared__ SMem sm; stage45(p, &sm, blockIdx.x, gridDim.x, threadIdx.x, 1); }
+__global__ __launch_bounds__(256) void k_s6(P p) { __shared__ SMem sm; stage6(p, &sm, blockIdx.x, gridDim.x, threadIdx.x); }
+__global__ void k_s7(P p) { stage7(p, (long)blockIdx.x * 256 + threadIdx.x, (long)gridDim.x * 256); }
 
 extern "C" void kernel_launch(void* const* d_in, const int* in_sizes, int n_in,
                               void* d_out, int out_size, void* d_ws, size_t ws_size,
@@ -540,62 +557,65 @@
     return (void*)(ws + o);
   };
 
-  int* ctrl = (int*)alloc(16);
-  float* stats = (float*)alloc(2560 * 4);
+  P p;
+  p.ctrl = (int*)alloc(16);
+  p.stats = (float*)alloc(2560 * 4);
   size_t fill_beg = off;
-  int* idx0 = (int*)alloc((size_t)B_ * D0_ * HW_ * 4);
-  int* idx1 = (int*)alloc((size_t)B_ * D1_ * HW_ * 4);
-  int* claim2 = (int*)alloc((size_t)B_ * D2_ * HW_ * 4);
+  p.idx0 = (int*)alloc((size_t)B_ * D0_ * HW_ * 4);
+  p.idx1 = (int*)alloc((size_t)B_ * D1_ * HW_ * 4);
+  p.claim2 = (int*)alloc((size_t)B_ * D2_ * HW_ * 4);
   size_t fill_end = off;
-  int* nbr1 = (int*)alloc((size_t)(ng1 + 4) * 432 * 4);
-  u32* gmask1 = (u32*)alloc((size_t)(ng1 + 4) * 4);
-  int* nbrz1 = (int*)alloc((size_t)cap1 * 3 * 4);
-  int* nbrz2 = (int*)alloc((size_t)cap2 * 3 * 4);
-  int* coords1 = (int*)alloc((size_t)cap1 * 4 * 4);
-  int* coords2 = (int*)alloc((size_t)cap2 * 4 * 4);
-  float* xb0 = (float*)alloc((size_t)N * 64 * 4);
-  float* xb1 = (float*)alloc((size_t)cap1 * 64 * 4);
-  float* xb2 = (float*)alloc((size_t)cap1 * 64 * 4);
-  float* xb3 = (float*)alloc((size_t)cap1 * 64 * 4);
-  float* xb4 = (float*)alloc((size_t)cap2 * 64 * 4);
-  u16* fb = (u16*)alloc((size_t)N * 128 * 2);
-  u16* wf0 = (u16*)alloc((size_t)27 * 4 * 2048 * 2);
-  u16* wf1a = (u16*)alloc((size_t)27 * 2 * 2048 * 2);
-  u16* wf1b = (u16*)alloc((size_t)27 * 2 * 2048 * 2);
-  u16* wfz1 = (u16*)alloc((size_t)3 * 2 * 2048 * 2);
-  u16* wfz2 = (u16*)alloc((size_t)3 * 2 * 2048 * 2);
-
-  const int* coors = (const int*)d_in[1];
-  auto gr = [](long n) { return dim3((unsigned)((n + 255) / 256)); };
-
-  int nfill16 = (int)((fill_end - fill_beg) / 16);
-  k_boot1<<<gr((long)nfill16 + 2563), 256, 0, stream>>>(ctrl, stats,
-                                                        (uint4*)(ws + fill_beg), nfill16, N);
-  long prepTotal = (long)N * 128 + 221184 + 110592 + 110592 + 12288 + 12288 + N;
-  k_boot2<<<gr(prepTotal), 256, 0, stream>>>((const float*)d_in[0], (const float*)d_in[3],
-                                             (const float*)d_in[9], (const float*)d_in[12],
-                                             (const float*)d_in[6], (const float*)d_in[15],
-                                             coors, fb, wf0, wf1a, wf1b, wfz1, wfz2, idx0, N);
-  k_conv0<<<dim3((N + 63) / 64), 256, 0, stream>>>(fb, coors, idx0, wf0, xb0, N, stats + 0,
-                                                   idx1, coords1, nbrz1, ctrl + 1);
-  k_convz<<<dim3((cap1 + 63) / 64), 256, 0, stream>>>(
-      xb0, nbrz1, wfz1, stats + 0, ctrl + 0, (const float*)d_in[4], (const float*)d_in[5],
-      xb1, ctrl + 1, stats + 512,
-      coords1, idx1, D1_, nbr1, gmask1,
-      D2_, claim2, coords2, nbrz2, ctrl + 2);
-  k_conv1<<<dim3((cap1 + 63) / 64), 256, 0, stream>>>(
-      xb1, nbr1, gmask1, wf1a, stats + 512, ctrl + 1, (const float*)d_in[7],
-      (const float*)d_in[8], xb2, ctrl + 1, stats + 1024);
-  k_conv1<<<dim3((cap1 + 63) / 64), 256, 0, stream>>>(
-      xb2, nbr1, gmask1, wf1b, stats + 1024, ctrl + 1, (const float*)d_in[10],
-      (const float*)d_in[11], xb3, ctrl + 1, stats + 1536);
-  k_convz<<<dim3((cap2 + 63) / 64), 256, 0, stream>>>(
-      xb3, nbrz2, wfz2, stats + 1536, ctrl + 1, (const float*)d_in[13], (const float*)d_in[14],
-      xb4, ctrl + 2, stats + 2048,
-      nullptr, nullptr, 0, nullptr, nullptr,
-      0, nullptr, nullptr, nullptr, nullptr);
-  long outThreads = (long)B_ * 64 * D2_ * H_ * (W_ / 4);
-  k_output<<<gr(outThreads), 256, 0, stream>>>(xb4, ctrl + 2, stats + 2048,
-                                               (const float*)d_in[16], (const float*)d_in[17],
-                                               claim2, (float*)d_out);
-}
+  p.nbr1 = (int*)alloc((size_t)(ng1 + 4) * 432 * 4);
+  p.gmask1 = (u32*)alloc((size_t)(ng1 + 4) * 4);
+  p.nbrz1 = (int*)alloc((size_t)cap1 * 3 * 4);
+  p.nbrz2 = (int*)alloc((size_t)cap2 * 3 * 4);
+  p.coords1 = (int*)alloc((size_t)cap1 * 4 * 4);
+  p.coords2 = (int*)alloc((size_t)cap2 * 4 * 4);
+  p.xb0 = (float*)alloc((size_t)N * 64 * 4);
+  p.xb1 = (float*)alloc((size_t)cap1 * 64 * 4);
+  p.xb2 = (float*)alloc((size_t)cap1 * 64 * 4);
+  p.xb3 = (float*)alloc((size_t)cap1 * 64 * 4);
+  p.xb4 = (float*)alloc((size_t)cap2 * 64 * 4);
+  p.fb = (u16*)alloc((size_t)N * 128 * 2);
+  p.wf0 = (u16*)alloc((size_t)27 * 4 * 2048 * 2);
+  p.wf1a = (u16*)alloc((size_t)27 * 2 * 2048 * 2);
+  p.wf1b = (u16*)alloc((size_t)27 * 2 * 2048 * 2);
+  p.wfz1 = (u16*)alloc((size_t)3 * 2 * 2048 * 2);
+  p.wfz2 = (u16*)alloc((size_t)3 * 2 * 2048 * 2);
+
+  p.feats = (const float*)d_in[0];
+  p.coors = (const int*)d_in[1];
+  p.w0 = (const float*)d_in[3];
+  p.g0 = (const float*)d_in[4]; p.b0 = (const float*)d_in[5];
+  p.wz1 = (const float*)d_in[6];
+  p.g1 = (const float*)d_in[7]; p.b1 = (const float*)d_in[8];
+  p.w1a = (const float*)d_in[9];
+  p.g2 = (const float*)d_in[10]; p.b2 = (const float*)d_in[11];
+  p.w1b = (const float*)d_in[12];
+  p.g3 = (const float*)d_in[13]; p.b3 = (const float*)d_in[14];
+  p.wz2 = (const float*)d_in[15];
+  p.g4 = (const float*)d_in[16]; p.b4 = (const float*)d_in[17];
+  p.out = (float*)d_out;
+  p.fillp = (uint4*)(ws + fill_beg);
+  p.N = N;
+  p.nfill16 = (int)((fill_end - fill_beg) / 16);
+  p.prepTotal = (long)N * 128 + 221184 + 110592 + 110592 + 12288 + 12288 + N;
+
+  void* args[] = {&p};
+  hipError_t e = hipLaunchCooperativeKernel((const void*)k_mega, dim3(NBLK), dim3(256), args, 0,
+                                            stream);
+  if (e != hipSuccess) {
+    const int nb0 = (N + 63) / 64;
+    const int nb1 = (cap1 + 63) / 64;
+    const int nb2 = (cap2 + 63) / 64;
+    long outThreads = (long)B_ * 64 * D2_ * H_ * (W_ / 4);
+    k_s0<<<dim3(512), 256, 0, stream>>>(p);
+    k_s1<<<dim3((unsigned)((p.prepTotal + 255) / 256)), 256, 0, stream>>>(p);
+    k_s2<<<dim3(nb0), 256, 0, stream>>>(p);
+    k_s3<<<dim3(nb1), 256, 0, stream>>>(p);
+    k_s4<<<dim3(nb1), 256, 0, stream>>>(p);
+    k_s5<<<dim3(nb1), 256, 0, stream>>>(p);
+    k_s6<<<dim3(nb2), 256, 0, stream>>>(p);
+    k_s7<<<dim3((unsigned)((outThreads + 255) / 256)), 256, 0, stream>>>(p);
+  }
+}
```
